# Optimization experiments

Hardware: AMD Instinct MI355X
Metric: run time of the kernel (lower is better)

## Reference

```python
import jax, jax.numpy as jnp
import numpy as np

C_IN, C_KEY, C_VAL, C_OUT = 256, 128, 128, 256
B, H, W = 4, 64, 64
BN_EPS = 1e-5


def conv1x1(x, w, b):
    # x: [B,C,H,W], w: [O,C], b: [O]
    return jnp.einsum('bchw,oc->bohw', x, w) + b[None, :, None, None]


def bn_relu(x, gamma, beta, mean, var):
    inv = jax.lax.rsqrt(var + BN_EPS)
    y = (x - mean[None, :, None, None]) * (gamma * inv)[None, :, None, None] + beta[None, :, None, None]
    return jax.nn.relu(y)


def setup_inputs() -> dict:
    key = jax.random.key(0)
    ks = jax.random.split(key, 16)
    s = 0.05
    return {
        'x_enc': jax.random.normal(ks[0], (B, C_IN, H, W), jnp.float32),
        'x_dec': jax.random.normal(ks[1], (B, C_IN, H, W), jnp.float32),
        # f_key: conv + BN params
        'wk': jax.random.normal(ks[2], (C_KEY, C_IN), jnp.float32) * s,
        'bk': jax.random.normal(ks[3], (C_KEY,), jnp.float32) * s,
        'gk': jax.random.uniform(ks[4], (C_KEY,), jnp.float32, 0.5, 1.5),
        'betak': jax.random.normal(ks[5], (C_KEY,), jnp.float32) * s,
        'mk': jax.random.normal(ks[6], (C_KEY,), jnp.float32) * s,
        'vk': jax.random.uniform(ks[7], (C_KEY,), jnp.float32, 0.5, 1.5),
        # f_query: conv + BN params
        'wq': jax.random.normal(ks[8], (C_KEY, C_IN), jnp.float32) * s,
        'bq': jax.random.normal(ks[9], (C_KEY,), jnp.float32) * s,
        'gq': jax.random.uniform(ks[10], (C_KEY,), jnp.float32, 0.5, 1.5),
        'betaq': jax.random.normal(ks[11], (C_KEY,), jnp.float32) * s,
        'mq': jax.random.normal(ks[12], (C_KEY,), jnp.float32) * s,
        'vq': jax.random.uniform(ks[13], (C_KEY,), jnp.float32, 0.5, 1.5),
        # f_value conv
        'wv': jax.random.normal(ks[14], (C_VAL, C_IN), jnp.float32) * s,
        'bv': jnp.zeros((C_VAL,), jnp.float32),
        # output projection W (random instead of zero-init to avoid degenerate baseline)
        'wo': jax.random.normal(ks[15], (C_OUT, C_VAL), jnp.float32) * s,
        'bo': jnp.zeros((C_OUT,), jnp.float32),
    }


def reference(x_enc, x_dec, wk, bk, gk, betak, mk, vk, wq, bq, gq, betaq, mq, vq, wv, bv, wo, bo):
    b, _, h, w = x_enc.shape
    hw = h * w
    # value: [B, HW, Cv]
    value = conv1x1(x_enc, wv, bv).reshape(b, C_VAL, hw).transpose(0, 2, 1)
    # query: [B, HW, Ck]
    query = bn_relu(conv1x1(x_dec, wq, bq), gq, betaq, mq, vq).reshape(b, C_KEY, hw).transpose(0, 2, 1)
    # key: [B, Ck, HW]
    key = bn_relu(conv1x1(x_enc, wk, bk), gk, betak, mk, vk).reshape(b, C_KEY, hw)
    sim = jnp.einsum('bqc,bck->bqk', query, key) * (C_KEY ** -0.5)  # [B, HW, HW]
    attn = jax.nn.softmax(sim, axis=-1)
    context = jnp.einsum('bqk,bkc->bqc', attn, value)  # [B, HW, Cv]
    context = context.transpose(0, 2, 1).reshape(b, C_VAL, h, w)
    return conv1x1(context, wo, bo)
```

## Files before the change

### kernel.cpp

```cpp
#include <hip/hip_runtime.h>

typedef __attribute__((ext_vector_type(8))) short short8;
typedef __attribute__((ext_vector_type(4))) float floatx4;

#define HW 4096
#define CIN 256
#define CK 128
#define COUT 256
#define NB 4
#define BN_EPS 1e-5f
#define SC2 0.12751744526f

#define MFMA(a, b, c) __builtin_amdgcn_mfma_f32_16x16x32_bf16((a), (b), (c), 0, 0, 0)

__device__ __forceinline__ unsigned short f2bf(float f) {
  union { float f; unsigned u; } v; v.f = f;
  return (unsigned short)((v.u + 0x8000u) >> 16);
}

__device__ __forceinline__ unsigned pack2(float a, float b) {
  union { float f; unsigned u; } va, vb; va.f = a; vb.f = b;
  return __builtin_amdgcn_perm(vb.u + 0x8000u, va.u + 0x8000u, 0x07060302u);
}

__device__ __forceinline__ float bf2f(unsigned short u) {
  union { unsigned u; float f; } v; v.u = ((unsigned)u) << 16;
  return v.f;
}

__device__ __forceinline__ short8 pack8(const float* p) {
  union { unsigned u[4]; short8 s; } v;
  v.u[0] = pack2(p[0], p[1]);
  v.u[1] = pack2(p[2], p[3]);
  v.u[2] = pack2(p[4], p[5]);
  v.u[3] = pack2(p[6], p[7]);
  return v.s;
}

__global__ __launch_bounds__(256) void prep_kernel(
    const float* __restrict__ wq, const float* __restrict__ wk,
    const float* __restrict__ wv, const float* __restrict__ wo,
    unsigned short* __restrict__ WqP, unsigned short* __restrict__ WkvP,
    unsigned short* __restrict__ WoP)
{
  const int t = blockIdx.x * 256 + threadIdx.x;
  float tmp[8];
  if (t < 4096) {
    const int lane = t & 63, mt = (t >> 6) & 1, wave = (t >> 7) & 3, ks = t >> 9;
    const int lane16 = lane & 15, quad = lane >> 4;
    const int o = wave * 32 + mt * 16 + lane16;
    const float* src = wq + (size_t)o * CIN + ks * 32 + quad * 8;
    *(float4*)tmp = *(const float4*)src;
    *(float4*)(tmp + 4) = *(const float4*)(src + 4);
    *(short8*)&WqP[(size_t)t * 8] = pack8(tmp);
  } else if (t < 12288) {
    const int u = t - 4096;
    const int lane = u & 63, mt = (u >> 6) & 3, wave = (u >> 8) & 3, ks = u >> 10;
    const int lane16 = lane & 15, quad = lane >> 4;
    const int o = wave * 64 + mt * 16 + lane16;
    const float* row = (o < 128) ? wk + (size_t)o * CIN : wv + (size_t)(o - 128) * CIN;
    const float* src = row + ks * 32 + quad * 8;
    *(float4*)tmp = *(const float4*)src;
    *(float4*)(tmp + 4) = *(const float4*)(src + 4);
    *(short8*)&WkvP[(size_t)u * 8] = pack8(tmp);
  } else {
    const int u = t - 12288;
    const int lane = u & 63, mt = (u >> 6) & 3, wave = (u >> 8) & 3, ks = u >> 10;
    const int lane16 = lane & 15, quad = lane >> 4;
    const int o = wave * 64 + mt * 16 + lane16;
    const float* src = wo + (size_t)o * CK + ks * 32 + quad * 8;
    *(float4*)tmp = *(const float4*)src;
    *(float4*)(tmp + 4) = *(const float4*)(src + 4);
    *(short8*)&WoP[(size_t)u * 8] = pack8(tmp);
  }
}

__global__ __launch_bounds__(256) void proj_kernel(
    const float* __restrict__ x_enc, const float* __restrict__ x_dec,
    const unsigned short* __restrict__ WqP, const unsigned short* __restrict__ WkvP,
    const float* __restrict__ bq, const float* __restrict__ gq,
    const float* __restrict__ betaq, const float* __restrict__ mq,
    const float* __restrict__ vq,
    const float* __restrict__ bk, const float* __restrict__ gk,
    const float* __restrict__ betak, const float* __restrict__ mk,
    const float* __restrict__ vk, const float* __restrict__ bv,
    unsigned short* __restrict__ Qb, unsigned short* __restrict__ Kb,
    unsigned short* __restrict__ Vt)
{
  const int tid = threadIdx.x;
  const int pt = blockIdx.x;
  const int b  = blockIdx.y;
  const int pj = blockIdx.z;

  const float* X = (pj == 0) ? x_dec : x_enc;

  __shared__ float xF[64 * 68];
  __shared__ unsigned short xT[64 * 264];

  const float* Xs = X + (size_t)b * CIN * HW + (size_t)pt * 64;
#pragma unroll
  for (int qtr = 0; qtr < 4; ++qtr) {
    if (qtr) __syncthreads();
    {
      const int c = tid >> 2;
      const int p0 = (tid & 3) * 16;
      const float* src = Xs + (size_t)(qtr * 64 + c) * HW + p0;
#pragma unroll
      for (int j = 0; j < 4; ++j)
        *(float4*)&xF[c * 68 + p0 + j * 4] = *(const float4*)(src + j * 4);
    }
    __syncthreads();
    {
      const int p = tid & 63;
      const int cb = tid >> 6;
#pragma unroll
      for (int jj = 0; jj < 2; ++jj) {
        const int c0 = (jj * 4 + cb) * 8;
        float t[8];
#pragma unroll
        for (int u = 0; u < 8; ++u) t[u] = xF[(c0 + u) * 68 + p];
        *(short8*)&xT[p * 264 + qtr * 64 + c0] = pack8(t);
      }
    }
  }
  __syncthreads();

  const int wave = tid >> 6;
  const int lane = tid & 63;
  const int lane16 = lane & 15;
  const int quad = lane >> 4;

  if (pj == 0) {
    floatx4 acc[2][4];
#pragma unroll
    for (int mt = 0; mt < 2; ++mt)
#pragma unroll
      for (int nf = 0; nf < 4; ++nf) acc[mt][nf] = (floatx4){0.f, 0.f, 0.f, 0.f};

#pragma unroll
    for (int ks = 0; ks < 8; ++ks) {
      short8 af[2];
#pragma unroll
      for (int mt = 0; mt < 2; ++mt)
        af[mt] = *(const short8*)&WqP[(size_t)((((ks * 4 + wave) * 2 + mt) * 64) + lane) * 8];
#pragma unroll
      for (int nf = 0; nf < 4; ++nf) {
        const short8 bf = *(const short8*)&xT[(nf * 16 + lane16) * 264 + ks * 32 + quad * 8];
#pragma unroll
        for (int mt = 0; mt < 2; ++mt) acc[mt][nf] = MFMA(af[mt], bf, acc[mt][nf]);
      }
    }

    float sc[2][4], off[2][4];
#pragma unroll
    for (int mt = 0; mt < 2; ++mt)
#pragma unroll
      for (int r = 0; r < 4; ++r) {
        const int o = wave * 32 + mt * 16 + quad * 4 + r;
        const float s = gq[o] * rsqrtf(vq[o] + BN_EPS) * SC2;
        sc[mt][r] = s;
        off[mt][r] = (bq[o] - mq[o]) * s + betaq[o] * SC2;
      }
#pragma unroll
    for (int nf = 0; nf < 4; ++nf) {
      const size_t prow = ((size_t)b * HW + pt * 64 + nf * 16 + lane16) * CK;
#pragma unroll
      for (int mt = 0; mt < 2; ++mt) {
        const unsigned lo = pack2(fmaxf(acc[mt][nf][0] * sc[mt][0] + off[mt][0], 0.f),
                                  fmaxf(acc[mt][nf][1] * sc[mt][1] + off[mt][1], 0.f));
        const unsigned hi = pack2(fmaxf(acc[mt][nf][2] * sc[mt][2] + off[mt][2], 0.f),
                                  fmaxf(acc[mt][nf][3] * sc[mt][3] + off[mt][3], 0.f));
        *(uint2*)(Qb + prow + wave * 32 + mt * 16 + quad * 4) = make_uint2(lo, hi);
      }
    }
  } else {
    const bool isK = (wave < 2);
    floatx4 acc[4][4];
#pragma unroll
    for (int mt = 0; mt < 4; ++mt)
#pragma unroll
      for (int nf = 0; nf < 4; ++nf) acc[mt][nf] = (floatx4){0.f, 0.f, 0.f, 0.f};

#pragma unroll
    for (int ks = 0; ks < 8; ++ks) {
      short8 af[4];
#pragma unroll
      for (int mt = 0; mt < 4; ++mt)
        af[mt] = *(const short8*)&WkvP[(size_t)((((ks * 4 + wave) * 4 + mt) * 64) + lane) * 8];
#pragma unroll
      for (int nf = 0; nf < 4; ++nf) {
        const short8 bf = *(const short8*)&xT[(nf * 16 + lane16) * 264 + ks * 32 + quad * 8];
#pragma unroll
        for (int mt = 0; mt < 4; ++mt) acc[mt][nf] = MFMA(af[mt], bf, acc[mt][nf]);
      }
    }

    if (isK) {
      float sc[4][4], off[4][4];
#pragma unroll
      for (int mt = 0; mt < 4; ++mt)
#pragma unroll
        for (int r = 0; r < 4; ++r) {
          const int o = wave * 64 + mt * 16 + quad * 4 + r;
          const float s = gk[o] * rsqrtf(vk[o] + BN_EPS);
          sc[mt][r] = s;
          off[mt][r] = (bk[o] - mk[o]) * s + betak[o];
        }
#pragma unroll
      for (int nf = 0; nf < 4; ++nf) {
        const size_t prow = ((size_t)b * HW + pt * 64 + nf * 16 + lane16) * CK;
#pragma unroll
        for (int mt = 0; mt < 4; ++mt) {
          const unsigned lo = pack2(fmaxf(acc[mt][nf][0] * sc[mt][0] + off[mt][0], 0.f),
                                    fmaxf(acc[mt][nf][1] * sc[mt][1] + off[mt][1], 0.f));
          const unsigned hi = pack2(fmaxf(acc[mt][nf][2] * sc[mt][2] + off[mt][2], 0.f),
                                    fmaxf(acc[mt][nf][3] * sc[mt][3] + off[mt][3], 0.f));
          *(uint2*)(Kb + prow + wave * 64 + mt * 16 + quad * 4) = make_uint2(lo, hi);
        }
      }
    } else {
#pragma unroll
      for (int mt = 0; mt < 4; ++mt) {
#pragma unroll
        for (int r = 0; r < 4; ++r) {
          const int c = wave * 64 + mt * 16 + quad * 4 + r - 128;
          const float bias = bv[c];
          unsigned short* dst = Vt + ((size_t)(b * CK + c)) * HW + pt * 64;
#pragma unroll
          for (int nf = 0; nf < 4; ++nf)
            dst[nf * 16 + lane16] = f2bf(acc[mt][nf][r] + bias);
        }
      }
    }
  }
}

template<int NKC>
__global__ __launch_bounds__(512) void attn_kernel8(
    const unsigned short* __restrict__ Qb, const unsigned short* __restrict__ Kb,
    const unsigned short* __restrict__ Vt, unsigned short* __restrict__ OpartH,
    float* __restrict__ Ml)
{
  constexpr int ITERS = 64 / NKC;
  const int tid = threadIdx.x;
  const int blk = blockIdx.x;
  const int b  = blk & 3;
  const int qt = (blk >> 2) & 15;
  const int kc = blk >> 6;

  const int wave = tid >> 6;
  const int lane = tid & 63;
  const int lane16 = lane & 15;
  const int quad = lane >> 4;

  __shared__ unsigned short Kl[2][64 * 136];
  __shared__ unsigned short Vl[2][128 * 72];

  const int q0 = qt * 256 + wave * 32;
  short8 qf[2][4];
  {
    const unsigned short* Qs = Qb + ((size_t)b * HW + q0) * CK;
#pragma unroll
    for (int mt = 0; mt < 2; ++mt)
#pragma unroll
      for (int ks = 0; ks < 4; ++ks)
        qf[mt][ks] = *(const short8*)(Qs + (size_t)(mt * 16 + lane16) * CK + ks * 32 + quad * 8);
  }

  short8 ones;
#pragma unroll
  for (int i = 0; i < 8; ++i) ones[i] = (short)0x3F80;

  floatx4 O[2][8];
  floatx4 Lacc[2];
#pragma unroll
  for (int mt = 0; mt < 2; ++mt) {
    Lacc[mt] = (floatx4){0.f, 0.f, 0.f, 0.f};
#pragma unroll
    for (int nf = 0; nf < 8; ++nf) O[mt][nf] = (floatx4){0.f, 0.f, 0.f, 0.f};
  }

  const int krow = tid >> 4;
  const int kcol = (tid & 15) * 8;
  const int vrow = tid >> 2;
  const int vcol = (tid & 3) * 16;

  int kslot[2];
#pragma unroll
  for (int i2 = 0; i2 < 2; ++i2) {
    const int g = krow + i2 * 32;
    kslot[i2] = (g & 0x23) | ((g & 0x18) >> 1) | ((g & 0x04) << 2);
  }

  const unsigned short* Kg = Kb + ((size_t)b * HW + (size_t)kc * ITERS * 64) * CK;
  const unsigned short* Vg = Vt + (size_t)b * CK * HW + kc * ITERS * 64;

  short8 kr[2], vr[2];
#pragma unroll
  for (int i2 = 0; i2 < 2; ++i2)
    kr[i2] = *(const short8*)(Kg + (size_t)(krow + i2 * 32) * CK + kcol);
#pragma unroll
  for (int i2 = 0; i2 < 2; ++i2)
    vr[i2] = *(const short8*)(Vg + (size_t)vrow * HW + vcol + i2 * 8);

#pragma unroll
  for (int i2 = 0; i2 < 2; ++i2)
    *(short8*)&Kl[0][kslot[i2] * 136 + kcol] = kr[i2];
#pragma unroll
  for (int i2 = 0; i2 < 2; ++i2)
    *(short8*)&Vl[0][vrow * 72 + vcol + i2 * 8] = vr[i2];
  __syncthreads();

  for (int it = 0; it < ITERS; ++it) {
    const int cur = it & 1;
    const unsigned short* Klc = &Kl[cur][0];
    const unsigned short* Vlc = &Vl[cur][0];

    if (it + 1 < ITERS) {
      const unsigned short* Kn = Kg + (size_t)((it + 1) * 64) * CK;
      const unsigned short* Vn = Vg + (it + 1) * 64;
#pragma unroll
      for (int i2 = 0; i2 < 2; ++i2)
        kr[i2] = *(const short8*)(Kn + (size_t)(krow + i2 * 32) * CK + kcol);
#pragma unroll
      for (int i2 = 0; i2 < 2; ++i2)
        vr[i2] = *(const short8*)(Vn + (size_t)vrow * HW + vcol + i2 * 8);
    }

    __builtin_amdgcn_s_setprio(1);
#pragma unroll
    for (int kp = 0; kp < 2; ++kp) {
      floatx4 sA0 = (floatx4){0.f, 0.f, 0.f, 0.f};
      floatx4 sA1 = (floatx4){0.f, 0.f, 0.f, 0.f};
      floatx4 sB0 = (floatx4){0.f, 0.f, 0.f, 0.f};
      floatx4 sB1 = (floatx4){0.f, 0.f, 0.f, 0.f};
#pragma unroll
      for (int ks = 0; ks < 4; ++ks) {
        const short8 kfA = *(const short8*)&Klc[((2 * kp) * 16 + lane16) * 136 + ks * 32 + quad * 8];
        const short8 kfB = *(const short8*)&Klc[((2 * kp + 1) * 16 + lane16) * 136 + ks * 32 + quad * 8];
        sA0 = MFMA(kfA, qf[0][ks], sA0);
        sA1 = MFMA(kfA, qf[1][ks], sA1);
        sB0 = MFMA(kfB, qf[0][ks], sB0);
        sB1 = MFMA(kfB, qf[1][ks], sB1);
      }
      union { unsigned u[4]; short8 s; } pf0, pf1;
      pf0.u[0] = pack2(__builtin_amdgcn_exp2f(sA0[0]), __builtin_amdgcn_exp2f(sA0[1]));
      pf0.u[1] = pack2(__builtin_amdgcn_exp2f(sA0[2]), __builtin_amdgcn_exp2f(sA0[3]));
      pf0.u[2] = pack2(__builtin_amdgcn_exp2f(sB0[0]), __builtin_amdgcn_exp2f(sB0[1]));
      pf0.u[3] = pack2(__builtin_amdgcn_exp2f(sB0[2]), __builtin_amdgcn_exp2f(sB0[3]));
      pf1.u[0] = pack2(__builtin_amdgcn_exp2f(sA1[0]), __builtin_amdgcn_exp2f(sA1[1]));
      pf1.u[1] = pack2(__builtin_amdgcn_exp2f(sA1[2]), __builtin_amdgcn_exp2f(sA1[3]));
      pf1.u[2] = pack2(__builtin_amdgcn_exp2f(sB1[0]), __builtin_amdgcn_exp2f(sB1[1]));
      pf1.u[3] = pack2(__builtin_amdgcn_exp2f(sB1[2]), __builtin_amdgcn_exp2f(sB1[3]));

      Lacc[0] = MFMA(pf0.s, ones, Lacc[0]);
      Lacc[1] = MFMA(pf1.s, ones, Lacc[1]);
#pragma unroll
      for (int nf = 0; nf < 8; ++nf) {
        const short8 vf = *(const short8*)&Vlc[(nf * 16 + lane16) * 72 + kp * 32 + quad * 8];
        O[0][nf] = MFMA(pf0.s, vf, O[0][nf]);
        O[1][nf] = MFMA(pf1.s, vf, O[1][nf]);
      }
    }
    __builtin_amdgcn_s_setprio(0);

    if (it + 1 < ITERS) {
      const int nxt = cur ^ 1;
#pragma unroll
      for (int i2 = 0; i2 < 2; ++i2)
        *(short8*)&Kl[nxt][kslot[i2] * 136 + kcol] = kr[i2];
#pragma unroll
      for (int i2 = 0; i2 < 2; ++i2)
        *(short8*)&Vl[nxt][vrow * 72 + vcol + i2 * 8] = vr[i2];
    }
    __syncthreads();
  }

  const int qt128 = qt * 2 + (wave >> 2);
  const int w4 = wave & 3;
  const int chunk = (b * 32 + qt128) * NKC + kc;
  unsigned short* Op = OpartH + (size_t)chunk * (128 * 128);
#pragma unroll
  for (int mt = 0; mt < 2; ++mt)
#pragma unroll
    for (int nf = 0; nf < 8; ++nf)
#pragma unroll
      for (int r = 0; r < 4; ++r)
        Op[(size_t)(w4 * 32 + mt * 16 + quad * 4 + r) * 128 + nf * 16 + lane16] =
            f2bf(O[mt][nf][r]);
  if (lane16 == 0) {
    float* Mp = Ml + (size_t)chunk * 128 + w4 * 32;
#pragma unroll
    for (int mt = 0; mt < 2; ++mt)
#pragma unroll
      for (int r = 0; r < 4; ++r)
        Mp[mt * 16 + quad * 4 + r] = Lacc[mt][r];
  }
}

template<int NKC>
__global__ __launch_bounds__(256) void outproj_kernel(
    const unsigned short* __restrict__ OpartH, const float* __restrict__ Ml,
    const unsigned short* __restrict__ WoP, const float* __restrict__ bo,
    float* __restrict__ out)
{
  const int tid = threadIdx.x;
  const int pt = blockIdx.x;
  const int b  = blockIdx.y;
  const int qt = pt >> 3;
  const int q0 = (pt & 7) * 16;
  const int chunk0 = (b * 32 + qt) * NKC;

  __shared__ unsigned short Ctile[16 * 136];

  {
    const int row = tid >> 4;
    const int c8  = (tid & 15) * 8;
    float L = 0.f;
#pragma unroll
    for (int k = 0; k < NKC; ++k) L += Ml[(size_t)(chunk0 + k) * 128 + q0 + row];
    float acc[8];
#pragma unroll
    for (int i = 0; i < 8; ++i) acc[i] = 0.f;
#pragma unroll
    for (int k = 0; k < NKC; ++k) {
      const short8 v = *(const short8*)(OpartH + (size_t)(chunk0 + k) * 16384 +
                                        (size_t)(q0 + row) * 128 + c8);
#pragma unroll
      for (int i = 0; i < 8; ++i) acc[i] += bf2f((unsigned short)v[i]);
    }
    const float inv = 1.f / L;
#pragma unroll
    for (int i = 0; i < 8; ++i) acc[i] *= inv;
    *(short8*)&Ctile[row * 136 + c8] = pack8(acc);
  }
  __syncthreads();

  const int wave = tid >> 6;
  const int lane = tid & 63;
  const int lane16 = lane & 15;
  const int quad = lane >> 4;

  floatx4 acc[4];
#pragma unroll
  for (int mt = 0; mt < 4; ++mt) acc[mt] = (floatx4){0.f, 0.f, 0.f, 0.f};

#pragma unroll
  for (int ks = 0; ks < 4; ++ks) {
    const short8 bf = *(const short8*)&Ctile[lane16 * 136 + ks * 32 + quad * 8];
#pragma unroll
    for (int mt = 0; mt < 4; ++mt) {
      const short8 af = *(const short8*)&WoP[(size_t)((((ks * 4 + wave) * 4 + mt) * 64) + lane) * 8];
      acc[mt] = MFMA(af, bf, acc[mt]);
    }
  }

#pragma unroll
  for (int mt = 0; mt < 4; ++mt) {
#pragma unroll
    for (int r = 0; r < 4; ++r) {
      const int o = wave * 64 + mt * 16 + quad * 4 + r;
      float* dst = out + ((size_t)b * COUT + o) * HW + qt * 128 + q0;
      dst[lane16] = acc[mt][r] + bo[o];
    }
  }
}

extern "C" void kernel_launch(void* const* d_in, const int* in_sizes, int n_in,
                              void* d_out, int out_size, void* d_ws, size_t ws_size,
                              hipStream_t stream)
{
  (void)in_sizes; (void)n_in; (void)out_size;
  const float* x_enc = (const float*)d_in[0];
  const float* x_dec = (const float*)d_in[1];
  const float* wk    = (const float*)d_in[2];
  const float* bk    = (const float*)d_in[3];
  const float* gk    = (const float*)d_in[4];
  const float* betak = (const float*)d_in[5];
  const float* mk    = (const float*)d_in[6];
  const float* vk    = (const float*)d_in[7];
  const float* wq    = (const float*)d_in[8];
  const float* bq    = (const float*)d_in[9];
  const float* gq    = (const float*)d_in[10];
  const float* betaq = (const float*)d_in[11];
  const float* mq    = (const float*)d_in[12];
  const float* vq    = (const float*)d_in[13];
  const float* wv    = (const float*)d_in[14];
  const float* bv    = (const float*)d_in[15];
  const float* wo    = (const float*)d_in[16];
  const float* bo    = (const float*)d_in[17];
  float* out = (float*)d_out;

  const size_t qkv = (size_t)NB * HW * CK;
  unsigned short* WqP  = (unsigned short*)d_ws;
  unsigned short* WkvP = WqP + 32768;
  unsigned short* WoP  = WkvP + 65536;
  unsigned short* Qb   = WoP + 32768;
  unsigned short* Kb   = Qb + qkv;
  unsigned short* Vt   = Kb + qkv;
  unsigned short* OpartH = Vt + qkv;
  const size_t fixed_bytes = 131072 * 2 + 3 * qkv * 2;

  prep_kernel<<<dim3(64), 256, 0, stream>>>(wq, wk, wv, wo, WqP, WkvP, WoP);
  proj_kernel<<<dim3(64, 4, 2), 256, 0, stream>>>(
      x_enc, x_dec, WqP, WkvP,
      bq, gq, betaq, mq, vq, bk, gk, betak, mk, vk, bv, Qb, Kb, Vt);

  auto need = [&](int nkc) {
    return fixed_bytes + (size_t)128 * nkc * 16384 * 2
                       + (size_t)128 * nkc * 128 * 4;
  };
  if (ws_size >= need(8)) {
    float* Ml = (float*)(OpartH + (size_t)128 * 8 * 16384);
    attn_kernel8<8><<<dim3(512), 512, 0, stream>>>(Qb, Kb, Vt, OpartH, Ml);
    outproj_kernel<8><<<dim3(256, 4), 256, 0, stream>>>(OpartH, Ml, WoP, bo, out);
  } else if (ws_size >= need(4)) {
    float* Ml = (float*)(OpartH + (size_t)128 * 4 * 16384);
    attn_kernel8<4><<<dim3(256), 512, 0, stream>>>(Qb, Kb, Vt, OpartH, Ml);
    outproj_kernel<4><<<dim3(256, 4), 256, 0, stream>>>(OpartH, Ml, WoP, bo, out);
  } else if (ws_size >= need(2)) {
    float* Ml = (float*)(OpartH + (size_t)128 * 2 * 16384);
    attn_kernel8<2><<<dim3(128), 512, 0, stream>>>(Qb, Kb, Vt, OpartH, Ml);
    outproj_kernel<2><<<dim3(256, 4), 256, 0, stream>>>(OpartH, Ml, WoP, bo, out);
  } else {
    float* Ml = (float*)(OpartH + (size_t)128 * 1 * 16384);
    attn_kernel8<1><<<dim3(64), 512, 0, stream>>>(Qb, Kb, Vt, OpartH, Ml);
    outproj_kernel<1><<<dim3(256, 4), 256, 0, stream>>>(OpartH, Ml, WoP, bo, out);
  }
}
```

Before: 165.2 us.

## Drop weight-prep kernel and convert fp32 weights to bf16 inline; stagger waves' K-pass order

Removes the separate prep kernel that repacked weights into MFMA fragment layout as bf16. The projection and output-projection kernels now read fp32 weight rows directly and convert them to bf16 fragments in registers, which saves one launch and a workspace round-trip. In exchange every block reloads twice the weight bytes in a less coalesced pattern and repeats the conversion. The attention kernel also makes odd waves do the two key sub-passes in reverse order, which may spread contention on shared resources.

```diff
diff --git a/kernel.cpp b/kernel.cpp
--- a/kernel.cpp
+++ b/kernel.cpp
@@ -37,47 +37,21 @@
   return v.s;
 }
 
-__global__ __launch_bounds__(256) void prep_kernel(
-    const float* __restrict__ wq, const float* __restrict__ wk,
-    const float* __restrict__ wv, const float* __restrict__ wo,
-    unsigned short* __restrict__ WqP, unsigned short* __restrict__ WkvP,
-    unsigned short* __restrict__ WoP)
-{
-  const int t = blockIdx.x * 256 + threadIdx.x;
-  float tmp[8];
-  if (t < 4096) {
-    const int lane = t & 63, mt = (t >> 6) & 1, wave = (t >> 7) & 3, ks = t >> 9;
-    const int lane16 = lane & 15, quad = lane >> 4;
-    const int o = wave * 32 + mt * 16 + lane16;
-    const float* src = wq + (size_t)o * CIN + ks * 32 + quad * 8;
-    *(float4*)tmp = *(const float4*)src;
-    *(float4*)(tmp + 4) = *(const float4*)(src + 4);
-    *(short8*)&WqP[(size_t)t * 8] = pack8(tmp);
-  } else if (t < 12288) {
-    const int u = t - 4096;
-    const int lane = u & 63, mt = (u >> 6) & 3, wave = (u >> 8) & 3, ks = u >> 10;
-    const int lane16 = lane & 15, quad = lane >> 4;
-    const int o = wave * 64 + mt * 16 + lane16;
-    const float* row = (o < 128) ? wk + (size_t)o * CIN : wv + (size_t)(o - 128) * CIN;
-    const float* src = row + ks * 32 + quad * 8;
-    *(float4*)tmp = *(const float4*)src;
-    *(float4*)(tmp + 4) = *(const float4*)(src + 4);
-    *(short8*)&WkvP[(size_t)u * 8] = pack8(tmp);
-  } else {
-    const int u = t - 12288;
-    const int lane = u & 63, mt = (u >> 6) & 3, wave = (u >> 8) & 3, ks = u >> 10;
-    const int lane16 = lane & 15, quad = lane >> 4;
-    const int o = wave * 64 + mt * 16 + lane16;
-    const float* src = wo + (size_t)o * CK + ks * 32 + quad * 8;
-    *(float4*)tmp = *(const float4*)src;
-    *(float4*)(tmp + 4) = *(const float4*)(src + 4);
-    *(short8*)&WoP[(size_t)u * 8] = pack8(tmp);
-  }
+__device__ __forceinline__ short8 wfrag(const float* src) {
+  const float4 a0 = *(const float4*)src;
+  const float4 a1 = *(const float4*)(src + 4);
+  union { unsigned u[4]; short8 s; } v;
+  v.u[0] = pack2(a0.x, a0.y);
+  v.u[1] = pack2(a0.z, a0.w);
+  v.u[2] = pack2(a1.x, a1.y);
+  v.u[3] = pack2(a1.z, a1.w);
+  return v.s;
 }
 
 __global__ __launch_bounds__(256) void proj_kernel(
     const float* __restrict__ x_enc, const float* __restrict__ x_dec,
-    const unsigned short* __restrict__ WqP, const unsigned short* __restrict__ WkvP,
+    const float* __restrict__ wq, const float* __restrict__ wk,
+    const float* __restrict__ wv,
     const float* __restrict__ bq, const float* __restrict__ gq,
     const float* __restrict__ betaq, const float* __restrict__ mq,
     const float* __restrict__ vq,
@@ -141,8 +115,10 @@
     for (int ks = 0; ks < 8; ++ks) {
       short8 af[2];
 #pragma unroll
-      for (int mt = 0; mt < 2; ++mt)
-        af[mt] = *(const short8*)&WqP[(size_t)((((ks * 4 + wave) * 2 + mt) * 64) + lane) * 8];
+      for (int mt = 0; mt < 2; ++mt) {
+        const int o = wave * 32 + mt * 16 + lane16;
+        af[mt] = wfrag(wq + (size_t)o * CIN + ks * 32 + quad * 8);
+      }
 #pragma unroll
       for (int nf = 0; nf < 4; ++nf) {
         const short8 bf = *(const short8*)&xT[(nf * 16 + lane16) * 264 + ks * 32 + quad * 8];
@@ -185,8 +161,12 @@
     for (int ks = 0; ks < 8; ++ks) {
       short8 af[4];
 #pragma unroll
-      for (int mt = 0; mt < 4; ++mt)
-        af[mt] = *(const short8*)&WkvP[(size_t)((((ks * 4 + wave) * 4 + mt) * 64) + lane) * 8];
+      for (int mt = 0; mt < 4; ++mt) {
+        const int o = wave * 64 + mt * 16 + lane16;
+        const float* row = isK ? (wk + (size_t)o * CIN)
+                               : (wv + (size_t)(o - 128) * CIN);
+        af[mt] = wfrag(row + ks * 32 + quad * 8);
+      }
 #pragma unroll
       for (int nf = 0; nf < 4; ++nf) {
         const short8 bf = *(const short8*)&xT[(nf * 16 + lane16) * 264 + ks * 32 + quad * 8];
@@ -284,6 +264,7 @@
   const int kcol = (tid & 15) * 8;
   const int vrow = tid >> 2;
   const int vcol = (tid & 3) * 16;
+  const int kpo  = wave & 1;
 
   int kslot[2];
 #pragma unroll
@@ -329,7 +310,8 @@
 
     __builtin_amdgcn_s_setprio(1);
 #pragma unroll
-    for (int kp = 0; kp < 2; ++kp) {
+    for (int kp2 = 0; kp2 < 2; ++kp2) {
+      const int kp = kp2 ^ kpo;
       floatx4 sA0 = (floatx4){0.f, 0.f, 0.f, 0.f};
       floatx4 sA1 = (floatx4){0.f, 0.f, 0.f, 0.f};
       floatx4 sB0 = (floatx4){0.f, 0.f, 0.f, 0.f};
@@ -401,7 +383,7 @@
 template<int NKC>
 __global__ __launch_bounds__(256) void outproj_kernel(
     const unsigned short* __restrict__ OpartH, const float* __restrict__ Ml,
-    const unsigned short* __restrict__ WoP, const float* __restrict__ bo,
+    const float* __restrict__ wo, const float* __restrict__ bo,
     float* __restrict__ out)
 {
   const int tid = threadIdx.x;
@@ -450,7 +432,8 @@
     const short8 bf = *(const short8*)&Ctile[lane16 * 136 + ks * 32 + quad * 8];
 #pragma unroll
     for (int mt = 0; mt < 4; ++mt) {
-      const short8 af = *(const short8*)&WoP[(size_t)((((ks * 4 + wave) * 4 + mt) * 64) + lane) * 8];
+      const int o = wave * 64 + mt * 16 + lane16;
+      const short8 af = wfrag(wo + (size_t)o * CK + ks * 32 + quad * 8);
       acc[mt] = MFMA(af, bf, acc[mt]);
     }
   }
@@ -492,18 +475,14 @@
   float* out = (float*)d_out;
 
   const size_t qkv = (size_t)NB * HW * CK;
-  unsigned short* WqP  = (unsigned short*)d_ws;
-  unsigned short* WkvP = WqP + 32768;
-  unsigned short* WoP  = WkvP + 65536;
-  unsigned short* Qb   = WoP + 32768;
+  unsigned short* Qb   = (unsigned short*)d_ws;
   unsigned short* Kb   = Qb + qkv;
   unsigned short* Vt   = Kb + qkv;
   unsigned short* OpartH = Vt + qkv;
-  const size_t fixed_bytes = 131072 * 2 + 3 * qkv * 2;
-
-  prep_kernel<<<dim3(64), 256, 0, stream>>>(wq, wk, wv, wo, WqP, WkvP, WoP);
+  const size_t fixed_bytes = 3 * qkv * 2;
+
   proj_kernel<<<dim3(64, 4, 2), 256, 0, stream>>>(
-      x_enc, x_dec, WqP, WkvP,
+      x_enc, x_dec, wq, wk, wv,
       bq, gq, betaq, mq, vq, bk, gk, betak, mk, vk, bv, Qb, Kb, Vt);
 
   auto need = [&](int nkc) {
@@ -513,18 +492,18 @@
   if (ws_size >= need(8)) {
     float* Ml = (float*)(OpartH + (size_t)128 * 8 * 16384);
     attn_kernel8<8><<<dim3(512), 512, 0, stream>>>(Qb, Kb, Vt, OpartH, Ml);
-    outproj_kernel<8><<<dim3(256, 4), 256, 0, stream>>>(OpartH, Ml, WoP, bo, out);
+    outproj_kernel<8><<<dim3(256, 4), 256, 0, stream>>>(OpartH, Ml, wo, bo, out);
   } else if (ws_size >= need(4)) {
     float* Ml = (float*)(OpartH + (size_t)128 * 4 * 16384);
     attn_kernel8<4><<<dim3(256), 512, 0, stream>>>(Qb, Kb, Vt, OpartH, Ml);
-    outproj_kernel<4><<<dim3(256, 4), 256, 0, stream>>>(OpartH, Ml, WoP, bo, out);
+    outproj_kernel<4><<<dim3(256, 4), 256, 0, stream>>>(OpartH, Ml, wo, bo, out);
   } else if (ws_size >= need(2)) {
     float* Ml = (float*)(OpartH + (size_t)128 * 2 * 16384);
     attn_kernel8<2><<<dim3(128), 512, 0, stream>>>(Qb, Kb, Vt, OpartH, Ml);
-    outproj_kernel<2><<<dim3(256, 4), 256, 0, stream>>>(OpartH, Ml, WoP, bo, out);
+    outproj_kernel<2><<<dim3(256, 4), 256, 0, stream>>>(OpartH, Ml, wo, bo, out);
   } else {
     float* Ml = (float*)(OpartH + (size_t)128 * 1 * 16384);
     attn_kernel8<1><<<dim3(64), 512, 0, stream>>>(Qb, Kb, Vt, OpartH, Ml);
-    outproj_kernel<1><<<dim3(256, 4), 256, 0, stream>>>(OpartH, Ml, WoP, bo, out);
-  }
-}
+    outproj_kernel<1><<<dim3(256, 4), 256, 0, stream>>>(OpartH, Ml, wo, bo, out);
+  }
+}
```

Result: slower. 181.7 us (+10.0%).
